# Kernel tuning notes

Measured on AMD Instinct MI355X. Metric: run time of the kernel, lower is better.

The kernel has to match this reference:

```python
import jax, jax.numpy as jnp
import numpy as np

HIDDEN = 2048
CONNECTIVITY = 0.1
NNZ = int(HIDDEN * HIDDEN * CONNECTIVITY)  # 419430
BATCH, SEQ = 4, 2048


def setup_inputs() -> dict:
    key = jax.random.key(0)
    k1, k2, k3, k4 = jax.random.split(key, 4)
    x_current = jax.random.normal(k1, (BATCH, SEQ, HIDDEN), dtype=jnp.float32)
    x_prev = jax.random.normal(k2, (BATCH, SEQ, HIDDEN), dtype=jnp.float32)
    connection_indices = jax.random.randint(k3, (2, NNZ), 0, HIDDEN, dtype=jnp.int32)
    connection_values = jax.random.normal(k4, (NNZ,), dtype=jnp.float32) * 0.001
    alpha = jnp.float32(0.01)
    return {
        "x_current": x_current,
        "x_prev": x_prev,
        "alpha": alpha,
        "connection_values": connection_values,
        "connection_indices": connection_indices,
    }


def reference(x_current, x_prev, alpha, connection_values, connection_indices):
    H = x_current.shape[-1]
    # Dense W from COO; duplicates are summed (torch sparse_coo_tensor semantics).
    W = jnp.zeros((H, H), dtype=connection_values.dtype).at[
        connection_indices[0], connection_indices[1]
    ].add(connection_values)
    # lateral = x_prev @ W.T : out[b,s,i] = sum_j x_prev[b,s,j] * W[i,j]
    lateral = jnp.einsum("bsj,ij->bsi", x_prev, W)
    return x_current + alpha * lateral
```

## Files before the change

### kernel.cpp

```cpp
#include <hip/hip_runtime.h>
#include <hip/hip_bf16.h>

#define HIDDEN 2048
#define NT 16
#define LDS_BYTES 49152

typedef __attribute__((ext_vector_type(4))) float f32x4;
typedef __attribute__((ext_vector_type(4))) int   i32x4;
typedef __attribute__((ext_vector_type(8))) int   i32x8;

#define GLDS(gptr, lptr)                                                       \
    __builtin_amdgcn_global_load_lds(                                          \
        (const __attribute__((address_space(1))) void*)(gptr),                 \
        (__attribute__((address_space(3))) void*)(lptr), 16, 0, 0)

#define SCHED0() __builtin_amdgcn_sched_barrier(0)
#define BARRIER() __builtin_amdgcn_s_barrier()
#define LGKMC(n) do { asm volatile("s_waitcnt lgkmcnt(" #n ")" ::: "memory"); SCHED0(); } while (0)
#define VMCNT(n)  do { asm volatile("s_waitcnt vmcnt(" #n ")" ::: "memory"); SCHED0(); } while (0)
#define PRIO1() __builtin_amdgcn_s_setprio(1)
#define PRIO0() __builtin_amdgcn_s_setprio(0)

#define SCALE1 0x7F7F7F7F

#define MFMA4(a, b, c)                                                         \
    __builtin_amdgcn_mfma_scale_f32_16x16x128_f8f6f4(                          \
        (a), (b), (c), 4, 4, 0, SCALE1, 0, SCALE1)

__global__ void build_w_kernel(const float* __restrict__ vals,
                               const int* __restrict__ rows,
                               const int* __restrict__ cols,
                               float* __restrict__ W, int nnz) {
    int k = blockIdx.x * blockDim.x + threadIdx.x;
    if (k < nnz) atomicAdd(&W[(size_t)rows[k] * HIDDEN + cols[k]], vals[k]);
}

__device__ __forceinline__ unsigned q_e2m1(float x) {
    float v = fabsf(x);
    unsigned n;
    if      (v < 0.25f) n = 0;
    else if (v < 0.75f) n = 1;
    else if (v < 1.25f) n = 2;
    else if (v < 1.75f) n = 3;
    else if (v < 2.5f)  n = 4;
    else if (v < 3.5f)  n = 5;
    else if (v < 5.0f)  n = 6;
    else                n = 7;
    return n | (x < 0.0f ? 8u : 0u);
}

__global__ void convert_kernel(const float* __restrict__ xp,
                               unsigned int* __restrict__ xp4, int n8xp,
                               const float* __restrict__ W,
                               unsigned int* __restrict__ W4, int n8w) {
    int i = blockIdx.x * blockDim.x + threadIdx.x;
    const int stride = gridDim.x * blockDim.x;
    const int total = n8xp + n8w;
    for (; i < total; i += stride) {
        const bool isxp = (i < n8xp);
        const float* src = isxp ? xp : W;
        unsigned int* dst = isxp ? xp4 : W4;
        const float scale = isxp ? 1.0f : 1024.0f;
        const int j = isxp ? i : i - n8xp;
        f32x4 a = ((const f32x4*)src)[2 * j];
        f32x4 b = ((const f32x4*)src)[2 * j + 1];
        unsigned int w = 0;
        #pragma unroll
        for (int k = 0; k < 4; ++k) {
            w |= q_e2m1(a[k] * scale) << (4 * k);
            w |= q_e2m1(b[k] * scale) << (16 + 4 * k);
        }
        dst[j] = w;
    }
}

__global__ __launch_bounds__(512, 4) void gemm_kernel(
    const float* __restrict__ xc,
    const unsigned char* __restrict__ xp4,
    const unsigned char* __restrict__ w4,
    const float* __restrict__ alpha_p,
    float* __restrict__ out)
{
    extern __shared__ __align__(16) char lds[];

    const int tid  = threadIdx.x;
    const int lane = tid & 63;
    const int wave = tid >> 6;
    const int l15  = lane & 15;
    const int l4   = lane >> 4;

    const int xcd = blockIdx.x & 7;
    const int loc = blockIdx.x >> 3;
    const int m0  = (xcd * 4 + (loc >> 4)) * 256;
    const int n0  = (loc & 15) * 128;

    const int wm = (wave >> 1) * 64;
    const int wn = (wave & 1) * 64;

    const int srow = lane >> 2;
    const int sw   = (lane & 3) ^ ((srow >> 1) & 3);
    const unsigned char* const gA = xp4 + (size_t)(m0 + wave * 32 + srow) * 1024 + sw * 16;
    const unsigned char* const gB = w4  + (size_t)(n0 + wave * 16 + srow) * 1024 + sw * 16;

#define STAGE(t)                                                               \
    do {                                                                       \
        const int _t = (t);                                                    \
        if (_t < NT) {                                                         \
            const size_t _o = (size_t)_t * 64;                                 \
            char* const _dA = lds + (_t & 1) * 24576 + wave * 2048 + lane * 16;\
            char* const _dB = lds + (_t & 1) * 24576 + 16384 + wave * 1024 + lane * 16; \
            GLDS(gA + _o,          _dA);                                       \
            GLDS(gA + _o + 16384,  _dA + 1024);                  \
            GLDS(gB + _o,          _dB);                                       \
        }                                                                      \
    } while (0)

    const int kx   = (l4 ^ ((l15 >> 1) & 3)) * 16;
    const int rowb = l15 * 64;

#define LDFRAG(dst, base)                                                      \
    do {                                                                       \
        i32x4 _v = *(const i32x4*)((base) + rowb + kx);                        \
        (dst) = __builtin_shufflevector(_v, (i32x4){0, 0, 0, 0},               \
                                        0, 1, 2, 3, 4, 5, 6, 7);               \
    } while (0)

    f32x4 acc[4][4] = {};
    i32x8 a[4], b01[2], b23[2];

    STAGE(0);
    VMCNT(0);
    SCHED0(); BARRIER(); SCHED0();

    for (int tt = 0; tt < NT; ++tt) {
        const char* const Ab = lds + (tt & 1) * 24576 + wm * 64;
        const char* const Bb = lds + (tt & 1) * 24576 + 16384 + wn * 64;

        STAGE(tt + 1);
        SCHED0();

        #pragma unroll
        for (int mi = 0; mi < 4; ++mi)
            LDFRAG(a[mi], Ab + mi * 1024);
        #pragma unroll
        for (int nj = 0; nj < 2; ++nj)
            LDFRAG(b01[nj], Bb + nj * 1024);
        SCHED0();
        LGKMC(2);

        #pragma unroll
        for (int nj = 0; nj < 2; ++nj)
            LDFRAG(b23[nj], Bb + (2 + nj) * 1024);
        SCHED0();
        LGKMC(2);

        PRIO1();
        #pragma unroll
        for (int mi = 0; mi < 4; ++mi)
            #pragma unroll
            for (int nj = 0; nj < 2; ++nj)
                acc[mi][nj] = MFMA4(a[mi], b01[nj], acc[mi][nj]);
        PRIO0();
        SCHED0();
        LGKMC(0);

        PRIO1();
        #pragma unroll
        for (int mi = 0; mi < 4; ++mi)
            #pragma unroll
            for (int nj = 0; nj < 2; ++nj)
                acc[mi][2 + nj] = MFMA4(a[mi], b23[nj], acc[mi][2 + nj]);
        PRIO0();
        SCHED0();

        VMCNT(0);
        BARRIER(); SCHED0();
    }

    const float alpha = alpha_p[0] * (1.0f / 1024.0f);
    #pragma unroll
    for (int mi = 0; mi < 4; ++mi) {
        #pragma unroll
        for (int r = 0; r < 4; ++r) {
            const int m = m0 + wm + mi * 16 + l4 * 4 + r;
            #pragma unroll
            for (int nj = 0; nj < 4; ++nj) {
                const int n = n0 + wn + nj * 16 + l15;
                const size_t o = (size_t)m * HIDDEN + n;
                out[o] = xc[o] + alpha * acc[mi][nj][r];
            }
        }
    }
#undef STAGE
#undef LDFRAG
}

extern "C" void kernel_launch(void* const* d_in, const int* in_sizes, int n_in,
                              void* d_out, int out_size, void* d_ws, size_t ws_size,
                              hipStream_t stream) {
    const float* xc    = (const float*)d_in[0];
    const float* xp    = (const float*)d_in[1];
    const float* alpha = (const float*)d_in[2];
    const float* vals  = (const float*)d_in[3];
    const int*   idx   = (const int*)d_in[4];
    float* out = (float*)d_out;

    float*         W   = (float*)d_ws;
    unsigned char* W4  = (unsigned char*)((char*)d_ws + (16 << 20));
    unsigned char* xp4 = (unsigned char*)((char*)d_ws + (18 << 20));

    const int nnz = in_sizes[3];
    const int M   = in_sizes[0] / HIDDEN;

    (void)hipFuncSetAttribute((const void*)gemm_kernel,
                              hipFuncAttributeMaxDynamicSharedMemorySize, LDS_BYTES);

    hipMemsetAsync(W, 0, (size_t)HIDDEN * HIDDEN * sizeof(float), stream);
    build_w_kernel<<<(nnz + 255) / 256, 256, 0, stream>>>(vals, idx, idx + nnz, W, nnz);

    convert_kernel<<<2048, 256, 0, stream>>>(xp, (unsigned int*)xp4, in_sizes[1] / 8,
                                             W, (unsigned int*)W4, (HIDDEN * HIDDEN) / 8);

    dim3 grid((M / 256) * 16);
    gemm_kernel<<<grid, 512, LDS_BYTES, stream>>>(xc, xp4, W4, alpha, out);
}
```

Measured before the change: 83.75 us.

## Switch to 32x32x64 scaled fp4 MFMA and fuse W zeroing with xp quantization

Replaces the 16x16x128 scaled MFMA tiles with 32x32x64 tiles, reworking the LDS swizzle, fragment loads and epilogue indexing to match. This cuts the number of MFMA issues and LDS reads per tile. Preprocessing is reorganized: W is zeroed inside a prep kernel that also quantizes x_prev, and a separate kernel quantizes W after the scatter, replacing the memset. Output stores become nontemporal to avoid polluting cache.

```diff
diff --git a/kernel.cpp b/kernel.cpp
--- a/kernel.cpp
+++ b/kernel.cpp
@@ -5,9 +5,10 @@
 #define NT 16
 #define LDS_BYTES 49152
 
-typedef __attribute__((ext_vector_type(4))) float f32x4;
-typedef __attribute__((ext_vector_type(4))) int   i32x4;
-typedef __attribute__((ext_vector_type(8))) int   i32x8;
+typedef __attribute__((ext_vector_type(4)))  float f32x4;
+typedef __attribute__((ext_vector_type(16))) float f32x16;
+typedef __attribute__((ext_vector_type(4)))  int   i32x4;
+typedef __attribute__((ext_vector_type(8)))  int   i32x8;
 
 #define GLDS(gptr, lptr)                                                       \
     __builtin_amdgcn_global_load_lds(                                          \
@@ -23,9 +24,10 @@
 
 #define SCALE1 0x7F7F7F7F
 
-#define MFMA4(a, b, c)                                                         \
-    __builtin_amdgcn_mfma_scale_f32_16x16x128_f8f6f4(                          \
-        (a), (b), (c), 4, 4, 0, SCALE1, 0, SCALE1)
+#define EXT8(x) __builtin_shufflevector((x), (i32x4){0, 0, 0, 0}, 0, 1, 2, 3, 4, 5, 6, 7)
+#define MFMA32(a, b, c)                                                        \
+    __builtin_amdgcn_mfma_scale_f32_32x32x64_f8f6f4(                           \
+        EXT8(a), EXT8(b), (c), 4, 4, 0, SCALE1, 0, SCALE1)
 
 __global__ void build_w_kernel(const float* __restrict__ vals,
                                const int* __restrict__ rows,
@@ -49,28 +51,38 @@
     return n | (x < 0.0f ? 8u : 0u);
 }
 
-__global__ void convert_kernel(const float* __restrict__ xp,
-                               unsigned int* __restrict__ xp4, int n8xp,
-                               const float* __restrict__ W,
-                               unsigned int* __restrict__ W4, int n8w) {
-    int i = blockIdx.x * blockDim.x + threadIdx.x;
+__device__ __forceinline__ unsigned pack8_e2m1(const f32x4& a, const f32x4& b,
+                                               float scale) {
+    unsigned w = 0;
+    #pragma unroll
+    for (int k = 0; k < 4; ++k) {
+        w |= q_e2m1(a[k] * scale) << (4 * k);
+        w |= q_e2m1(b[k] * scale) << (16 + 4 * k);
+    }
+    return w;
+}
+
+__global__ void prep_kernel(float* __restrict__ W, int nW4,
+                            const float* __restrict__ xp,
+                            unsigned int* __restrict__ xp4, int n8xp) {
     const int stride = gridDim.x * blockDim.x;
-    const int total = n8xp + n8w;
-    for (; i < total; i += stride) {
-        const bool isxp = (i < n8xp);
-        const float* src = isxp ? xp : W;
-        unsigned int* dst = isxp ? xp4 : W4;
-        const float scale = isxp ? 1.0f : 1024.0f;
-        const int j = isxp ? i : i - n8xp;
-        f32x4 a = ((const f32x4*)src)[2 * j];
-        f32x4 b = ((const f32x4*)src)[2 * j + 1];
-        unsigned int w = 0;
-        #pragma unroll
-        for (int k = 0; k < 4; ++k) {
-            w |= q_e2m1(a[k] * scale) << (4 * k);
-            w |= q_e2m1(b[k] * scale) << (16 + 4 * k);
-        }
-        dst[j] = w;
+    const int i = blockIdx.x * blockDim.x + threadIdx.x;
+    for (int j = i; j < nW4; j += stride)
+        ((f32x4*)W)[j] = (f32x4){0.f, 0.f, 0.f, 0.f};
+    for (int j = i; j < n8xp; j += stride) {
+        f32x4 a = ((const f32x4*)xp)[2 * j];
+        f32x4 b = ((const f32x4*)xp)[2 * j + 1];
+        xp4[j] = pack8_e2m1(a, b, 1.0f);
+    }
+}
+
+__global__ void convw_kernel(const float* __restrict__ W,
+                             unsigned int* __restrict__ W4, int n8) {
+    const int stride = gridDim.x * blockDim.x;
+    for (int j = blockIdx.x * blockDim.x + threadIdx.x; j < n8; j += stride) {
+        f32x4 a = ((const f32x4*)W)[2 * j];
+        f32x4 b = ((const f32x4*)W)[2 * j + 1];
+        W4[j] = pack8_e2m1(a, b, 1024.0f);
     }
 }
 
@@ -86,8 +98,8 @@
     const int tid  = threadIdx.x;
     const int lane = tid & 63;
     const int wave = tid >> 6;
-    const int l15  = lane & 15;
-    const int l4   = lane >> 4;
+    const int l31  = lane & 31;
+    const int kh   = lane >> 5;
 
     const int xcd = blockIdx.x & 7;
     const int loc = blockIdx.x >> 3;
@@ -97,10 +109,17 @@
     const int wm = (wave >> 1) * 64;
     const int wn = (wave & 1) * 64;
 
-    const int srow = lane >> 2;
-    const int sw   = (lane & 3) ^ ((srow >> 1) & 3);
-    const unsigned char* const gA = xp4 + (size_t)(m0 + wave * 32 + srow) * 1024 + sw * 16;
-    const unsigned char* const gB = w4  + (size_t)(n0 + wave * 16 + srow) * 1024 + sw * 16;
+    const int lr = lane >> 2;
+    const int rA0 = lr;
+    const int rA1 = lr + 16;
+    const int rB  = ((wave & 1) * 16) + lr;
+    const int swA0 = (lane & 3) ^ ((rA0 >> 1) & 3) ^ ((rA0 >> 3) & 3);
+    const int swA1 = (lane & 3) ^ ((rA1 >> 1) & 3) ^ ((rA1 >> 3) & 3);
+    const int swB  = (lane & 3) ^ ((rB  >> 1) & 3) ^ ((rB  >> 3) & 3);
+
+    const unsigned char* const gA0 = xp4 + (size_t)(m0 + wave * 32 + lr)      * 1024 + swA0 * 16;
+    const unsigned char* const gA1 = xp4 + (size_t)(m0 + wave * 32 + 16 + lr) * 1024 + swA1 * 16;
+    const unsigned char* const gB  = w4  + (size_t)(n0 + wave * 16 + lr)      * 1024 + swB  * 16;
 
 #define STAGE(t)                                                               \
     do {                                                                       \
@@ -109,24 +128,19 @@
             const size_t _o = (size_t)_t * 64;                                 \
             char* const _dA = lds + (_t & 1) * 24576 + wave * 2048 + lane * 16;\
             char* const _dB = lds + (_t & 1) * 24576 + 16384 + wave * 1024 + lane * 16; \
-            GLDS(gA + _o,          _dA);                                       \
-            GLDS(gA + _o + 16384,  _dA + 1024);                  \
-            GLDS(gB + _o,          _dB);                                       \
+            GLDS(gA0 + _o, _dA);                                               \
+            GLDS(gA1 + _o, _dA + 1024);                                       \
+            GLDS(gB  + _o, _dB);                                               \
         }                                                                      \
     } while (0)
 
-    const int kx   = (l4 ^ ((l15 >> 1) & 3)) * 16;
-    const int rowb = l15 * 64;
-
-#define LDFRAG(dst, base)                                                      \
-    do {                                                                       \
-        i32x4 _v = *(const i32x4*)((base) + rowb + kx);                        \
-        (dst) = __builtin_shufflevector(_v, (i32x4){0, 0, 0, 0},               \
-                                        0, 1, 2, 3, 4, 5, 6, 7);               \
-    } while (0)
-
-    f32x4 acc[4][4] = {};
-    i32x8 a[4], b01[2], b23[2];
+    const int swzr = ((l31 >> 1) & 3) ^ ((l31 >> 3) & 3);
+    const int kx0  = ((0 + kh) ^ swzr) * 16;
+    const int kx1  = ((2 + kh) ^ swzr) * 16;
+    const int rowb = l31 * 64;
+
+    f32x16 acc[2][2] = {};
+    i32x4 a0[2], a1[2], b0[2], b1[2];
 
     STAGE(0);
     VMCNT(0);
@@ -140,36 +154,37 @@
         SCHED0();
 
         #pragma unroll
-        for (int mi = 0; mi < 4; ++mi)
-            LDFRAG(a[mi], Ab + mi * 1024);
+        for (int mi = 0; mi < 2; ++mi)
+            a0[mi] = *(const i32x4*)(Ab + mi * 2048 + rowb + kx0);
         #pragma unroll
         for (int nj = 0; nj < 2; ++nj)
-            LDFRAG(b01[nj], Bb + nj * 1024);
-        SCHED0();
-        LGKMC(2);
-
+            b0[nj] = *(const i32x4*)(Bb + nj * 2048 + rowb + kx0);
+        SCHED0();
+        #pragma unroll
+        for (int mi = 0; mi < 2; ++mi)
+            a1[mi] = *(const i32x4*)(Ab + mi * 2048 + rowb + kx1);
         #pragma unroll
         for (int nj = 0; nj < 2; ++nj)
-            LDFRAG(b23[nj], Bb + (2 + nj) * 1024);
-        SCHED0();
-        LGKMC(2);
+            b1[nj] = *(const i32x4*)(Bb + nj * 2048 + rowb + kx1);
+        SCHED0();
+        LGKMC(4);
 
         PRIO1();
         #pragma unroll
-        for (int mi = 0; mi < 4; ++mi)
+        for (int mi = 0; mi < 2; ++mi)
             #pragma unroll
             for (int nj = 0; nj < 2; ++nj)
-                acc[mi][nj] = MFMA4(a[mi], b01[nj], acc[mi][nj]);
+                acc[mi][nj] = MFMA32(a0[mi], b0[nj], acc[mi][nj]);
         PRIO0();
         SCHED0();
         LGKMC(0);
 
         PRIO1();
         #pragma unroll
-        for (int mi = 0; mi < 4; ++mi)
+        for (int mi = 0; mi < 2; ++mi)
             #pragma unroll
             for (int nj = 0; nj < 2; ++nj)
-                acc[mi][2 + nj] = MFMA4(a[mi], b23[nj], acc[mi][2 + nj]);
+                acc[mi][nj] = MFMA32(a1[mi], b1[nj], acc[mi][nj]);
         PRIO0();
         SCHED0();
 
@@ -179,20 +194,19 @@
 
     const float alpha = alpha_p[0] * (1.0f / 1024.0f);
     #pragma unroll
-    for (int mi = 0; mi < 4; ++mi) {
-        #pragma unroll
-        for (int r = 0; r < 4; ++r) {
-            const int m = m0 + wm + mi * 16 + l4 * 4 + r;
+    for (int mi = 0; mi < 2; ++mi) {
+        #pragma unroll
+        for (int r = 0; r < 16; ++r) {
+            const int m = m0 + wm + mi * 32 + (r & 3) + 8 * (r >> 2) + 4 * kh;
             #pragma unroll
-            for (int nj = 0; nj < 4; ++nj) {
-                const int n = n0 + wn + nj * 16 + l15;
+            for (int nj = 0; nj < 2; ++nj) {
+                const int n = n0 + wn + nj * 32 + l31;
                 const size_t o = (size_t)m * HIDDEN + n;
-                out[o] = xc[o] + alpha * acc[mi][nj][r];
+                __builtin_nontemporal_store(xc[o] + alpha * acc[mi][nj][r], &out[o]);
             }
         }
     }
 #undef STAGE
-#undef LDFRAG
 }
 
 extern "C" void kernel_launch(void* const* d_in, const int* in_sizes, int n_in,
@@ -215,11 +229,10 @@
     (void)hipFuncSetAttribute((const void*)gemm_kernel,
                               hipFuncAttributeMaxDynamicSharedMemorySize, LDS_BYTES);
 
-    hipMemsetAsync(W, 0, (size_t)HIDDEN * HIDDEN * sizeof(float), stream);
+    prep_kernel<<<2048, 256, 0, stream>>>(W, (HIDDEN * HIDDEN) / 4,
+                                          xp, (unsigned int*)xp4, in_sizes[1] / 8);
     build_w_kernel<<<(nnz + 255) / 256, 256, 0, stream>>>(vals, idx, idx + nnz, W, nnz);
-
-    convert_kernel<<<2048, 256, 0, stream>>>(xp, (unsigned int*)xp4, in_sizes[1] / 8,
-                                             W, (unsigned int*)W4, (HIDDEN * HIDDEN) / 8);
+    convw_kernel<<<1024, 256, 0, stream>>>(W, (unsigned int*)W4, (HIDDEN * HIDDEN) / 8);
 
     dim3 grid((M / 256) * 16);
     gemm_kernel<<<grid, 512, LDS_BYTES, stream>>>(xc, xp4, W4, alpha, out);
```

Measured after the change: 81.69 us. 1.03x faster.
